# Kernel optimization log

Hardware: AMD Instinct MI355X
Metric: run time of the kernel (lower is better)

The kernel has to match this reference:

```python
import jax, jax.numpy as jnp
import numpy as np

N, S, D, H = 2048, 16, 128, 8
EPS = 1e-5  # torch.nn.LayerNorm default eps


def setup_inputs() -> dict:
    key = jax.random.key(0)
    ks = jax.random.split(key, 3)
    return {
        "x": jax.random.normal(ks[0], (N, S, D), jnp.float32),
        "Wi": jax.random.normal(ks[1], (H, S, D, D), jnp.float32),
        "Wj": jax.random.normal(ks[2], (H, S, 2 * D, D), jnp.float32),
        "ln1_w": jnp.ones((S, D), jnp.float32),
        "ln1_b": jnp.zeros((S, D), jnp.float32),
        "prelu1_a": jnp.float32(0.25),  # torch PReLU default single param
        "ln2_w": jnp.ones((H, D), jnp.float32),
        "ln2_b": jnp.zeros((H, D), jnp.float32),
        "prelu2_a": jnp.float32(0.25),
    }


def _layernorm2(x, w, b):
    # LayerNorm over the last two dims (matches torch LayerNorm([A, B]))
    mu = jnp.mean(x, axis=(-2, -1), keepdims=True)
    var = jnp.var(x, axis=(-2, -1), keepdims=True)
    return (x - mu) * jax.lax.rsqrt(var + EPS) * w + b


def _prelu(x, a):
    return jnp.where(x >= 0, x, a * x)


def reference(x, Wi, Wj, ln1_w, ln1_b, prelu1_a, ln2_w, ln2_b, prelu2_a):
    n, s, d = x.shape
    h = Wi.shape[0]
    # sort descending along source dim
    idx = jnp.argsort(-x, axis=1)                      # [N,S,D] int
    x_sort = jnp.take_along_axis(x, idx, axis=1)       # [N,S,D]
    # pad with a zero row, take adjacent differences
    pad = jnp.concatenate([x_sort, jnp.zeros((n, 1, d), x.dtype)], axis=1)
    diff = pad[:, :-1, :] - pad[:, 1:, :]              # [N,S,D]
    # positional encoding: cumsum of 2^rank / 2^S
    enc = jnp.cumsum(jnp.exp2(idx.astype(x.dtype)), axis=1) / jnp.asarray(2.0 ** s, x.dtype)
    # per-head, per-source batched matmul with Wi
    se = jnp.einsum('bsd,hsdo->bhso', enc, Wi)         # [N,H,S,D]
    se = _prelu(_layernorm2(se, ln1_w, ln1_b), prelu1_a)  # Dropout in eval mode = identity
    cat = jnp.concatenate(
        [jnp.broadcast_to(diff[:, None, :, :], (n, h, s, d)), se], axis=-1
    )                                                  # [N,H,S,2D]
    out = jnp.einsum('bhsd,hsdo->bho', cat, Wj)        # [N,H,D]
    return _prelu(_layernorm2(out, ln2_w, ln2_b), prelu2_a)
```

## Files before the change

kernel.cpp:

```cpp
#include <hip/hip_runtime.h>

#define N_ 2048
#define S_ 16
#define D_ 128
#define H_ 8
#define EPS_ 1e-5f

typedef unsigned short ushortT;
typedef unsigned int uint32;
typedef __attribute__((ext_vector_type(8))) short short8;
typedef __attribute__((ext_vector_type(8))) unsigned short ushort8;
typedef __attribute__((ext_vector_type(4))) float f32x4;
typedef __attribute__((ext_vector_type(4))) unsigned int uint4v;
typedef __attribute__((ext_vector_type(8))) float float8;

__device__ __forceinline__ ushortT f2bf(float f) {
  union { float f; uint32 u; } c; c.f = f;
  uint32 u = c.u;
  u = (u + 0x7FFFu + ((u >> 16) & 1u)) >> 16;
  return (ushortT)u;
}
__device__ __forceinline__ float bf2f(ushortT b) {
  union { uint32 u; float f; } c; c.u = ((uint32)b) << 16;
  return c.f;
}

__global__ __launch_bounds__(256) void k_prep(const float* __restrict__ x,
                                              ushortT* __restrict__ enc_sw,
                                              ushortT* __restrict__ diff_sw) {
  int g = blockIdx.x * 256 + threadIdx.x;
  int n = g >> 7, d = g & 127;
  const float* xp = x + (size_t)n * (S_ * D_) + d;
  float v[S_];
#pragma unroll
  for (int s = 0; s < S_; ++s) v[s] = xp[s * D_];
  int r[S_];
#pragma unroll
  for (int i = 0; i < S_; ++i) {
    int ri = 0;
#pragma unroll
    for (int j = 0; j < S_; ++j)
      ri += ((v[j] > v[i]) || (v[j] == v[i] && j < i)) ? 1 : 0;
    r[i] = ri;
  }
  float xs[S_ + 1];
#pragma unroll
  for (int s = 0; s < S_; ++s) {
    float acc = 0.f;
#pragma unroll
    for (int i = 0; i < S_; ++i) acc += (r[i] == s) ? v[i] : 0.f;
    xs[s] = acc;
  }
  xs[S_] = 0.f;
  int btq = n >> 7, row = n & 127;
  int wv = row >> 5, ii = (row >> 4) & 1, l15n = row & 15;
  int kkm = d >> 5, lgm = (d >> 3) & 3, em = d & 7;
  int off_nd = (((kkm * 2 + ii) * 64) + (l15n * 4 + lgm)) * 8 + em;
  int pp = d >> 6, c8p = (d >> 3) & 7, ee = d & 7;
  int q = row * 8 + (c8p ^ (row & 7));
#pragma unroll
  for (int s = 0; s < S_; ++s) {
    uint32 mm = 0;
#pragma unroll
    for (int i = 0; i < S_; ++i) mm |= (r[i] <= s) ? (1u << i) : 0u;
    enc_sw[(size_t)((btq * 16 + s) * 4 + wv) * 4096 + off_nd] =
        f2bf((float)mm * (1.f / 65536.f));
    size_t idx = ((((size_t)(btq * 16 + s) * 2 + pp) * 1024) + q) * 8 + ee;
    diff_sw[idx] = f2bf(xs[s] - xs[s + 1]);
  }
}

__global__ __launch_bounds__(512) void k_castW(const float* __restrict__ Wi,
                                               const float* __restrict__ Wj,
                                               ushortT* __restrict__ Wit_sw,
                                               ushortT* __restrict__ Wjt_sw) {
  __shared__ ushortT tile[128 * 136];
  int bx = blockIdx.x;
  int t = threadIdx.x;
  if (bx < 128) {
    int hs = bx;
    const float* src = Wi + (size_t)hs * D_ * D_;
#pragma unroll 4
    for (int i = 0; i < 32; ++i) {
      int e = t + 512 * i;
      int dd = e >> 7, o = e & 127;
      tile[dd * 136 + o] = f2bf(src[e]);
    }
    __syncthreads();
    ushortT* dst = Wit_sw + (size_t)hs * 16384;
#pragma unroll
    for (int r8 = 0; r8 < 4; ++r8) {
      int qc = r8 * 512 + t;
      int o = qc >> 4;
      int cc = (qc & 15) ^ (o & 7);
      uint4v pk;
#pragma unroll
      for (int w = 0; w < 4; ++w) {
        int d0 = cc * 8 + w * 2;
        ushortT lo = tile[d0 * 136 + o];
        ushortT hi = tile[(d0 + 1) * 136 + o];
        pk[w] = (uint32)lo | ((uint32)hi << 16);
      }
      *(uint4v*)(dst + qc * 8) = pk;
    }
  } else {
    int hs = bx - 128;
    const float* src = Wj + (size_t)hs * 256 * D_;
    for (int half = 0; half < 2; ++half) {
      if (half) __syncthreads();
#pragma unroll 4
      for (int i = 0; i < 32; ++i) {
        int e = t + 512 * i;
        int dd = e >> 7, o = e & 127;
        tile[dd * 136 + o] = f2bf(src[half * 16384 + e]);
      }
      __syncthreads();
      ushortT* dstb = Wjt_sw + ((size_t)hs * 4 + half * 2) * 8192;
#pragma unroll
      for (int r8 = 0; r8 < 4; ++r8) {
        int cg = r8 * 512 + t;
        int pl = cg >> 10;
        int qc = cg & 1023;
        int o = qc >> 3;
        int c8 = (qc & 7) ^ (o & 7);
        int dl = pl * 64 + c8 * 8;
        uint4v pk;
#pragma unroll
        for (int w = 0; w < 4; ++w) {
          ushortT lo = tile[(dl + w * 2) * 136 + o];
          ushortT hi = tile[(dl + w * 2 + 1) * 136 + o];
          pk[w] = (uint32)lo | ((uint32)hi << 16);
        }
        *(uint4v*)(dstb + (size_t)pl * 8192 + qc * 8) = pk;
      }
    }
  }
}

__global__ __launch_bounds__(256, 3) void k_gemm1(const ushortT* __restrict__ enc_sw,
                                                  const ushortT* __restrict__ Wit_sw,
                                                  ushortT* __restrict__ se,
                                                  float* __restrict__ ssum,
                                                  float* __restrict__ ssq) {
  int bt = blockIdx.x, s = blockIdx.y, h = blockIdx.z;
  __shared__ ushortT Bs[128 * 132];
  int tid = threadIdx.x;
  int wave = tid >> 6, lane = tid & 63;
  int l15 = lane & 15, lg = lane >> 4;

  const ushortT* bsrc = Wit_sw + (size_t)(h * 16 + s) * 16384;
#pragma unroll
  for (int r8 = 0; r8 < 8; ++r8)
    __builtin_amdgcn_global_load_lds(
        (const __attribute__((address_space(1))) void*)(bsrc + (r8 * 256 + tid) * 8),
        (__attribute__((address_space(3))) void*)(Bs + (r8 * 256 + wave * 64) * 8),
        16, 0, 0);

  short8 afr[4][2];
  const ushortT* abase = enc_sw + ((size_t)(bt * 16 + s) * 4 + wave) * 4096;
#pragma unroll
  for (int kk = 0; kk < 4; ++kk)
#pragma unroll
    for (int i = 0; i < 2; ++i)
      afr[kk][i] = *(const short8*)(abase + (((kk * 2 + i) * 64) + (l15 * 4 + lg)) * 8);

  __syncthreads();

  f32x4 acc[2][8];
#pragma unroll
  for (int i = 0; i < 2; ++i)
#pragma unroll
    for (int j = 0; j < 8; ++j) acc[i][j] = (f32x4)(0.f);
#pragma unroll
  for (int kk = 0; kk < 4; ++kk) {
    int cc = kk * 4 + lg;
    short8 b[8];
#pragma unroll
    for (int j = 0; j < 8; ++j) {
      int row = j * 16 + l15;
      b[j] = *(const short8*)(Bs + (row * 16 + (cc ^ (row & 7))) * 8);
    }
#pragma unroll
    for (int i = 0; i < 2; ++i)
#pragma unroll
      for (int j = 0; j < 8; ++j)
        acc[i][j] = __builtin_amdgcn_mfma_f32_16x16x32_bf16(afr[kk][i], b[j], acc[i][j], 0, 0, 0);
  }
#pragma unroll
  for (int i = 0; i < 2; ++i)
#pragma unroll
    for (int rr = 0; rr < 4; ++rr) {
      int rloc = wave * 32 + i * 16 + lg * 4 + rr;
      int b_g = bt * 128 + rloc;
      float rs = 0.f, rq = 0.f;
#pragma unroll
      for (int j = 0; j < 8; ++j) {
        float val = acc[i][j][rr];
        rs += val; rq += val * val;
      }
#pragma unroll
      for (int m = 1; m <= 8; m <<= 1) {
        rs += __shfl_xor(rs, m);
        rq += __shfl_xor(rq, m);
      }
      if (l15 == 0) {
        ssum[((size_t)s * N_ + b_g) * H_ + h] = rs;
        ssq[((size_t)s * N_ + b_g) * H_ + h] = rq;
      }
    }
  __syncthreads();
#pragma unroll
  for (int i = 0; i < 2; ++i)
#pragma unroll
    for (int rr = 0; rr < 4; ++rr) {
      int row = wave * 32 + i * 16 + lg * 4 + rr;
      int sw = (row & 7) << 3;
#pragma unroll
      for (int j = 0; j < 8; ++j) {
        int o = j * 16 + l15;
        Bs[row * 132 + (o ^ sw)] = f2bf(acc[i][j][rr]);
      }
    }
  __syncthreads();
#pragma unroll
  for (int p = 0; p < 2; ++p) {
    int row = p * 64 + (tid >> 2);
    int sw = (row & 7) << 3;
    int b_g = bt * 128 + row;
    ushortT* dst = se + (((size_t)b_g * H_ + h) * S_ + s) * D_;
#pragma unroll
    for (int qq = 0; qq < 4; ++qq) {
      int o0 = (qq * 4 + (tid & 3)) * 8;
      *(uint4v*)(dst + o0) = *(const uint4v*)(Bs + row * 132 + (o0 ^ sw));
    }
  }
}

__global__ __launch_bounds__(256) void k_finalize(const float* __restrict__ ssum,
                                                  const float* __restrict__ ssq,
                                                  float* __restrict__ mr) {
  int t = blockIdx.x * 256 + threadIdx.x;
  float s1 = 0.f, s2 = 0.f;
#pragma unroll
  for (int s = 0; s < S_; ++s) {
    s1 += ssum[(size_t)s * (N_ * H_) + t];
    s2 += ssq[(size_t)s * (N_ * H_) + t];
  }
  float mu = s1 * (1.f / 2048.f);
  float var = s2 * (1.f / 2048.f) - mu * mu;
  float rstd = rsqrtf(var + EPS_);
  mr[t * 2] = rstd;
  mr[t * 2 + 1] = -mu * rstd;
}

#define GLDS_B(DST, SRC) do {                                                 \
    const ushortT* sp_ = (SRC) + wave * 512 + lane * 8;                       \
    ushortT* dp_ = (DST) + wave * 512;                                        \
    _Pragma("unroll")                                                         \
    for (int i_ = 0; i_ < 4; ++i_)                                            \
      __builtin_amdgcn_global_load_lds(                                       \
          (const __attribute__((address_space(1))) void*)(sp_ + i_ * 2048),   \
          (__attribute__((address_space(3))) void*)(dp_ + i_ * 2048),         \
          16, 0, 0);                                                          \
  } while (0)

#define GLDS_A(DST, SRC) do {                                                 \
    const ushortT* sp_ = (SRC) + wave * 512 + lane * 8;                       \
    ushortT* dp_ = (DST) + wave * 512;                                        \
    _Pragma("unroll")                                                         \
    for (int i_ = 0; i_ < 2; ++i_)                                            \
      __builtin_amdgcn_global_load_lds(                                       \
          (const __attribute__((address_space(1))) void*)(sp_ + i_ * 2048),   \
          (__attribute__((address_space(3))) void*)(dp_ + i_ * 2048),         \
          16, 0, 0);                                                          \
  } while (0)

__global__ __launch_bounds__(256, 3) void k_gemm2(const ushortT* __restrict__ diff_sw,
                                                  const ushortT* __restrict__ se,
                                                  const ushortT* __restrict__ Wjt_sw,
                                                  const float* __restrict__ mr,
                                                  const float* __restrict__ ln1w,
                                                  const float* __restrict__ ln1b,
                                                  const float* __restrict__ pa1,
                                                  float* __restrict__ outp) {
  int bt2 = blockIdx.x, sh = blockIdx.y, h = blockIdx.z;
  int s0 = sh * 8;
  __shared__ ushortT As[2][64 * 64];
  __shared__ ushortT Bs[2][128 * 64];
  int tid = threadIdx.x;
  int wave = tid >> 6, lane = tid & 63;
  int c8 = tid & 7, trow = tid >> 3;
  int swst = ((c8 ^ (trow & 7)) * 8);
  int l15 = lane & 15, lg = lane >> 4;
  int wm = wave >> 1, wn = wave & 1;
  float a1 = pa1[0];

  float rs_r[2], nm_r[2];
  uint32 aoff_s[2];
#pragma unroll
  for (int i = 0; i < 2; ++i) {
    int row = i * 32 + trow;
    int b_g = bt2 * 64 + row;
    rs_r[i] = mr[((size_t)b_g * H_ + h) * 2];
    nm_r[i] = mr[((size_t)b_g * H_ + h) * 2 + 1];
    aoff_s[i] = ((uint32)b_g * H_ + h) * (S_ * D_) + c8 * 8;
  }
  const ushortT* dbase = diff_sw + (size_t)(bt2 >> 1) * (S_ * 2 * 8192) + (bt2 & 1) * 4096;
  ushort8 raL[2], raH[2];
  f32x4 acc[2][4];
#pragma unroll
  for (int i = 0; i < 2; ++i)
#pragma unroll
    for (int j = 0; j < 4; ++j) acc[i][j] = (f32x4)(0.f);

#define COMPUTE(XBUF) do {                                                    \
    _Pragma("unroll")                                                         \
    for (int kk = 0; kk < 2; ++kk) {                                          \
      int cc = kk * 4 + lg;                                                   \
      short8 a[2], b[4];                                                      \
      _Pragma("unroll")                                                       \
      for (int i = 0; i < 2; ++i) {                                           \
        int row = wm * 32 + i * 16 + l15;                                     \
        a[i] = *(const short8*)(As[XBUF] + row * 64 + ((cc ^ (row & 7)) * 8));\
      }                                                                       \
      _Pragma("unroll")                                                       \
      for (int j = 0; j < 4; ++j) {                                           \
        int row = wn * 64 + j * 16 + l15;                                     \
        b[j] = *(const short8*)(Bs[XBUF] + row * 64 + ((cc ^ (row & 7)) * 8));\
      }                                                                       \
      __builtin_amdgcn_s_setprio(1);                                          \
      _Pragma("unroll")                                                       \
      for (int i = 0; i < 2; ++i)                                             \
        _Pragma("unroll")                                                     \
        for (int j = 0; j < 4; ++j)                                           \
          acc[i][j] = __builtin_amdgcn_mfma_f32_16x16x32_bf16(a[i], b[j],     \
                                                              acc[i][j], 0, 0, 0); \
      __builtin_amdgcn_s_setprio(0);                                          \
    } } while (0)

#define TRANSFORM_WRITE(RA, NXBUF, SS, HALF) do {                             \
    float8 w8 = *(const float8*)(ln1w + (SS) * D_ + (HALF) * 64 + c8 * 8);    \
    float8 b8 = *(const float8*)(ln1b + (SS) * D_ + (HALF) * 64 + c8 * 8);    \
    _Pragma("unroll")                                                         \
    for (int i = 0; i < 2; ++i) {                                             \
      int row = i * 32 + trow;                                                \
      float y[8];                                                             \
      _Pragma("unroll")                                                       \
      for (int e = 0; e < 8; ++e) {                                           \
        float f = bf2f((ushortT)RA[i][e]);                                    \
        float tt = fmaf(f, rs_r[i], nm_r[i]);                                 \
        float vv = fmaf(tt, w8[e], b8[e]);                                    \
        y[e] = fmaf(a1, fminf(vv, 0.f), fmaxf(vv, 0.f));                      \
      }                                                                       \
      uint4v pk;                                                              \
      _Pragma("unroll")                                                       \
      for (int q = 0; q < 4; ++q) {                                           \
        uint32 rpk;                                                           \
        asm("v_cvt_pk_bf16_f32 %0, %1, %2" : "=v"(rpk)                        \
            : "v"(y[2 * q]), "v"(y[2 * q + 1]));                              \
        pk[q] = rpk;                                                          \
      }                                                                       \
      *(uint4v*)(As[NXBUF] + row * 64 + swst) = pk;                           \
    } } while (0)

  GLDS_A(As[0], dbase + ((size_t)s0 * 2 + 0) * 8192);
  GLDS_B(Bs[0], Wjt_sw + ((size_t)(h * 16 + s0) * 4 + 0) * 8192);
  __syncthreads();

  for (int si = 0; si < 8; ++si) {
    int s = s0 + si;
    int sn = (s + 1 < S_) ? s + 1 : 0;
#pragma unroll
    for (int i = 0; i < 2; ++i)
      raL[i] = *(const ushort8*)(se + aoff_s[i] + s * D_);
    GLDS_A(As[1], dbase + ((size_t)s * 2 + 1) * 8192);
    GLDS_B(Bs[1], Wjt_sw + ((size_t)(h * 16 + s) * 4 + 1) * 8192);
    COMPUTE(0);
    __syncthreads();
#pragma unroll
    for (int i = 0; i < 2; ++i)
      raH[i] = *(const ushort8*)(se + aoff_s[i] + s * D_ + 64);
    TRANSFORM_WRITE(raL, 0, s, 0);
    GLDS_B(Bs[0], Wjt_sw + ((size_t)(h * 16 + s) * 4 + 2) * 8192);
    COMPUTE(1);
    __syncthreads();
    TRANSFORM_WRITE(raH, 1, s, 1);
    GLDS_B(Bs[1], Wjt_sw + ((size_t)(h * 16 + s) * 4 + 3) * 8192);
    COMPUTE(0);
    __syncthreads();
    GLDS_A(As[0], dbase + ((size_t)sn * 2 + 0) * 8192);
    GLDS_B(Bs[0], Wjt_sw + ((size_t)(h * 16 + sn) * 4 + 0) * 8192);
    COMPUTE(1);
    __syncthreads();
  }

#pragma unroll
  for (int i = 0; i < 2; ++i)
#pragma unroll
    for (int j = 0; j < 4; ++j)
#pragma unroll
      for (int rr = 0; rr < 4; ++rr) {
        int b_g = bt2 * 64 + wm * 32 + i * 16 + lg * 4 + rr;
        int o = wn * 64 + j * 16 + l15;
        outp[(((size_t)sh * N_ + b_g) * H_ + h) * D_ + o] = acc[i][j][rr];
      }
}

__global__ __launch_bounds__(256) void k_ln2(const float* __restrict__ outp,
                                             const float* __restrict__ ln2w,
                                             const float* __restrict__ ln2b,
                                             const float* __restrict__ pa2,
                                             float* __restrict__ out) {
  int b = blockIdx.x, t = threadIdx.x;
  __shared__ float red[8];
  __shared__ float stats[2];
  f32x4 v = *((const f32x4*)(outp + (size_t)b * 1024) + t) +
            *((const f32x4*)(outp + (size_t)N_ * 1024 + (size_t)b * 1024) + t);
  float s1 = v[0] + v[1] + v[2] + v[3];
  float s2 = v[0] * v[0] + v[1] * v[1] + v[2] * v[2] + v[3] * v[3];
#pragma unroll
  for (int m = 1; m <= 32; m <<= 1) {
    s1 += __shfl_xor(s1, m);
    s2 += __shfl_xor(s2, m);
  }
  int wave = t >> 6, lane = t & 63;
  if (lane == 0) { red[wave] = s1; red[4 + wave] = s2; }
  __syncthreads();
  if (t == 0) {
    float S = red[0] + red[1] + red[2] + red[3];
    float Q = red[4] + red[5] + red[6] + red[7];
    float mu = S * (1.f / 1024.f);
    float var = Q * (1.f / 1024.f) - mu * mu;
    stats[0] = mu; stats[1] = rsqrtf(var + EPS_);
  }
  __syncthreads();
  float mu = stats[0], rstd = stats[1];
  float a2 = pa2[0];
  f32x4 wv = *((const f32x4*)ln2w + t);
  f32x4 bv = *((const f32x4*)ln2b + t);
  f32x4 r;
#pragma unroll
  for (int e = 0; e < 4; ++e) {
    float y = (v[e] - mu) * rstd * wv[e] + bv[e];
    r[e] = (y >= 0.f) ? y : a2 * y;
  }
  *((f32x4*)(out + (size_t)b * 1024) + t) = r;
}

extern "C" void kernel_launch(void* const* d_in, const int* in_sizes, int n_in,
                              void* d_out, int out_size, void* d_ws, size_t ws_size,
                              hipStream_t stream) {
  const float* x    = (const float*)d_in[0];
  const float* Wi   = (const float*)d_in[1];
  const float* Wj   = (const float*)d_in[2];
  const float* ln1w = (const float*)d_in[3];
  const float* ln1b = (const float*)d_in[4];
  const float* pa1  = (const float*)d_in[5];
  const float* ln2w = (const float*)d_in[6];
  const float* ln2b = (const float*)d_in[7];
  const float* pa2  = (const float*)d_in[8];
  char* ws = (char*)d_ws;
  ushortT* se      = (ushortT*)(ws + 0);
  ushortT* diff_sw = (ushortT*)(ws + 67108864);
  ushortT* Wjt_sw  = (ushortT*)(ws + 75497472);
  float*   outp    = (float*)(ws + 83886080);
  ushortT* enc_sw  = (ushortT*)(ws + 100663296);
  ushortT* Wit_sw  = (ushortT*)(ws + 109051904);
  float*   ssum    = (float*)(ws + 113246208);
  float*   ssq     = (float*)(ws + 114294784);
  float*   mr      = (float*)(ws + 115343360);
  float*   out     = (float*)d_out;

  hipLaunchKernelGGL(k_prep, dim3(1024), dim3(256), 0, stream, x, enc_sw, diff_sw);
  hipLaunchKernelGGL(k_castW, dim3(256), dim3(512), 0, stream, Wi, Wj, Wit_sw, Wjt_sw);
  hipLaunchKernelGGL(k_gemm1, dim3(16, 16, 8), dim3(256), 0, stream, enc_sw, Wit_sw, se, ssum, ssq);
  hipLaunchKernelGGL(k_finalize, dim3(64), dim3(256), 0, stream, ssum, ssq, mr);
  hipLaunchKernelGGL(k_gemm2, dim3(32, 2, 8), dim3(256), 0, stream, diff_sw, se, Wjt_sw, mr,
                     ln1w, ln1b, pa1, outp);
  hipLaunchKernelGGL(k_ln2, dim3(2048), dim3(256), 0, stream, outp, ln2w, ln2b, pa2, out);
}
```

Baseline: 183.4 us.

## Register-prefetch gemm2 operands and split S reduction into four partitions

The gemm2 kernel stops using direct global-to-LDS loads. It now prefetches the A/B tiles into registers several stages ahead and writes them to LDS after the previous compute step, which deepens the software pipeline. The source dimension is split four ways instead of two, doubling the grid to raise occupancy and parallelism. The cost is more partial-sum traffic: k_ln2 now reads four partials, and the workspace is relaid out to fit them. The register-staged buffers raise register pressure, which may limit occupancy under launch_bounds(256,3).

```diff
diff --git a/kernel.cpp b/kernel.cpp
--- a/kernel.cpp
+++ b/kernel.cpp
@@ -253,28 +253,6 @@
   mr[t * 2 + 1] = -mu * rstd;
 }
 
-#define GLDS_B(DST, SRC) do {                                                 \
-    const ushortT* sp_ = (SRC) + wave * 512 + lane * 8;                       \
-    ushortT* dp_ = (DST) + wave * 512;                                        \
-    _Pragma("unroll")                                                         \
-    for (int i_ = 0; i_ < 4; ++i_)                                            \
-      __builtin_amdgcn_global_load_lds(                                       \
-          (const __attribute__((address_space(1))) void*)(sp_ + i_ * 2048),   \
-          (__attribute__((address_space(3))) void*)(dp_ + i_ * 2048),         \
-          16, 0, 0);                                                          \
-  } while (0)
-
-#define GLDS_A(DST, SRC) do {                                                 \
-    const ushortT* sp_ = (SRC) + wave * 512 + lane * 8;                       \
-    ushortT* dp_ = (DST) + wave * 512;                                        \
-    _Pragma("unroll")                                                         \
-    for (int i_ = 0; i_ < 2; ++i_)                                            \
-      __builtin_amdgcn_global_load_lds(                                       \
-          (const __attribute__((address_space(1))) void*)(sp_ + i_ * 2048),   \
-          (__attribute__((address_space(3))) void*)(dp_ + i_ * 2048),         \
-          16, 0, 0);                                                          \
-  } while (0)
-
 __global__ __launch_bounds__(256, 3) void k_gemm2(const ushortT* __restrict__ diff_sw,
                                                   const ushortT* __restrict__ se,
                                                   const ushortT* __restrict__ Wjt_sw,
@@ -284,7 +262,7 @@
                                                   const float* __restrict__ pa1,
                                                   float* __restrict__ outp) {
   int bt2 = blockIdx.x, sh = blockIdx.y, h = blockIdx.z;
-  int s0 = sh * 8;
+  int s0 = sh * 4;
   __shared__ ushortT As[2][64 * 64];
   __shared__ ushortT Bs[2][128 * 64];
   int tid = threadIdx.x;
@@ -306,7 +284,76 @@
     aoff_s[i] = ((uint32)b_g * H_ + h) * (S_ * D_) + c8 * 8;
   }
   const ushortT* dbase = diff_sw + (size_t)(bt2 >> 1) * (S_ * 2 * 8192) + (bt2 & 1) * 4096;
-  ushort8 raL[2], raH[2];
+  const ushortT* wbase = Wjt_sw + (size_t)(h * 16) * 4 * 8192 + wave * 512 + lane * 8;
+
+  uint4v S0b0, S0b1, S0b2, S0b3, S0a0, S0a1;
+  uint4v S1b0, S1b1, S1b2, S1b3, S1a0, S1a1;
+  uint4v S2b0, S2b1, S2b2, S2b3, S2a0, S2a1;
+  uint4v S3b0, S3b1, S3b2, S3b3, S3a0, S3a1;
+
+#define ISSUE_B(P, SS, PP) do {                                               \
+    const ushortT* bp_ = wbase + ((size_t)(SS) * 4 + (PP)) * 8192;            \
+    P##b0 = *(const uint4v*)(bp_);                                            \
+    P##b1 = *(const uint4v*)(bp_ + 2048);                                     \
+    P##b2 = *(const uint4v*)(bp_ + 4096);                                     \
+    P##b3 = *(const uint4v*)(bp_ + 6144);                                     \
+  } while (0)
+
+#define ISSUE_DIFF(P, SS, PP) do {                                            \
+    ISSUE_B(P, SS, (PP));                                                     \
+    const ushortT* ap_ = dbase + ((size_t)(SS) * 2 + (PP)) * 8192 + wave * 512 + lane * 8; \
+    P##a0 = *(const uint4v*)(ap_);                                            \
+    P##a1 = *(const uint4v*)(ap_ + 2048);                                     \
+  } while (0)
+
+#define ISSUE_SE(P, SS, HALF) do {                                            \
+    ISSUE_B(P, SS, 2 + (HALF));                                               \
+    P##a0 = *(const uint4v*)(se + aoff_s[0] + (SS) * D_ + (HALF) * 64);       \
+    P##a1 = *(const uint4v*)(se + aoff_s[1] + (SS) * D_ + (HALF) * 64);       \
+  } while (0)
+
+#define WRITE_B(P, BUF) do {                                                  \
+    ushortT* dp_ = Bs[BUF] + wave * 512 + lane * 8;                           \
+    *(uint4v*)(dp_) = P##b0;                                                  \
+    *(uint4v*)(dp_ + 2048) = P##b1;                                           \
+    *(uint4v*)(dp_ + 4096) = P##b2;                                           \
+    *(uint4v*)(dp_ + 6144) = P##b3;                                           \
+  } while (0)
+
+#define WRITE_DIFF(P, BUF) do {                                               \
+    WRITE_B(P, BUF);                                                          \
+    ushortT* ap_ = As[BUF] + wave * 512 + lane * 8;                           \
+    *(uint4v*)(ap_) = P##a0;                                                  \
+    *(uint4v*)(ap_ + 2048) = P##a1;                                           \
+  } while (0)
+
+#define WRITE_SE(P, BUF, SS, HALF) do {                                       \
+    WRITE_B(P, BUF);                                                          \
+    float8 w8 = *(const float8*)(ln1w + (SS) * D_ + (HALF) * 64 + c8 * 8);    \
+    float8 b8 = *(const float8*)(ln1b + (SS) * D_ + (HALF) * 64 + c8 * 8);    \
+    _Pragma("unroll")                                                         \
+    for (int i_ = 0; i_ < 2; ++i_) {                                          \
+      ushort8 va_ = (i_ == 0) ? *(ushort8*)&P##a0 : *(ushort8*)&P##a1;        \
+      int row_ = i_ * 32 + trow;                                              \
+      float y_[8];                                                            \
+      _Pragma("unroll")                                                       \
+      for (int e_ = 0; e_ < 8; ++e_) {                                        \
+        float f_ = bf2f((ushortT)va_[e_]);                                    \
+        float t_ = fmaf(f_, rs_r[i_], nm_r[i_]);                              \
+        float v_ = fmaf(t_, w8[e_], b8[e_]);                                  \
+        y_[e_] = fmaf(a1, fminf(v_, 0.f), fmaxf(v_, 0.f));                    \
+      }                                                                       \
+      uint4v pk_;                                                             \
+      _Pragma("unroll")                                                       \
+      for (int q_ = 0; q_ < 4; ++q_) {                                        \
+        uint32 r_;                                                            \
+        asm("v_cvt_pk_bf16_f32 %0, %1, %2" : "=v"(r_)                         \
+            : "v"(y_[2 * q_]), "v"(y_[2 * q_ + 1]));                          \
+        pk_[q_] = r_;                                                         \
+      }                                                                       \
+      *(uint4v*)(As[BUF] + row_ * 64 + swst) = pk_;                           \
+    } } while (0)
+
   f32x4 acc[2][4];
 #pragma unroll
   for (int i = 0; i < 2; ++i)
@@ -338,58 +385,29 @@
       __builtin_amdgcn_s_setprio(0);                                          \
     } } while (0)
 
-#define TRANSFORM_WRITE(RA, NXBUF, SS, HALF) do {                             \
-    float8 w8 = *(const float8*)(ln1w + (SS) * D_ + (HALF) * 64 + c8 * 8);    \
-    float8 b8 = *(const float8*)(ln1b + (SS) * D_ + (HALF) * 64 + c8 * 8);    \
-    _Pragma("unroll")                                                         \
-    for (int i = 0; i < 2; ++i) {                                             \
-      int row = i * 32 + trow;                                                \
-      float y[8];                                                             \
-      _Pragma("unroll")                                                       \
-      for (int e = 0; e < 8; ++e) {                                           \
-        float f = bf2f((ushortT)RA[i][e]);                                    \
-        float tt = fmaf(f, rs_r[i], nm_r[i]);                                 \
-        float vv = fmaf(tt, w8[e], b8[e]);                                    \
-        y[e] = fmaf(a1, fminf(vv, 0.f), fmaxf(vv, 0.f));                      \
-      }                                                                       \
-      uint4v pk;                                                              \
-      _Pragma("unroll")                                                       \
-      for (int q = 0; q < 4; ++q) {                                           \
-        uint32 rpk;                                                           \
-        asm("v_cvt_pk_bf16_f32 %0, %1, %2" : "=v"(rpk)                        \
-            : "v"(y[2 * q]), "v"(y[2 * q + 1]));                              \
-        pk[q] = rpk;                                                          \
-      }                                                                       \
-      *(uint4v*)(As[NXBUF] + row * 64 + swst) = pk;                           \
-    } } while (0)
-
-  GLDS_A(As[0], dbase + ((size_t)s0 * 2 + 0) * 8192);
-  GLDS_B(Bs[0], Wjt_sw + ((size_t)(h * 16 + s0) * 4 + 0) * 8192);
+  ISSUE_DIFF(S0, s0, 0);
+  ISSUE_DIFF(S1, s0, 1);
+  ISSUE_SE(S2, s0, 0);
+  WRITE_DIFF(S0, 0);
   __syncthreads();
 
-  for (int si = 0; si < 8; ++si) {
+  for (int si = 0; si < 4; ++si) {
     int s = s0 + si;
-    int sn = (s + 1 < S_) ? s + 1 : 0;
-#pragma unroll
-    for (int i = 0; i < 2; ++i)
-      raL[i] = *(const ushort8*)(se + aoff_s[i] + s * D_);
-    GLDS_A(As[1], dbase + ((size_t)s * 2 + 1) * 8192);
-    GLDS_B(Bs[1], Wjt_sw + ((size_t)(h * 16 + s) * 4 + 1) * 8192);
+    int sn = (si + 1 < 4) ? s + 1 : s0;
+    ISSUE_SE(S3, s, 1);
+    WRITE_DIFF(S1, 1);
     COMPUTE(0);
     __syncthreads();
-#pragma unroll
-    for (int i = 0; i < 2; ++i)
-      raH[i] = *(const ushort8*)(se + aoff_s[i] + s * D_ + 64);
-    TRANSFORM_WRITE(raL, 0, s, 0);
-    GLDS_B(Bs[0], Wjt_sw + ((size_t)(h * 16 + s) * 4 + 2) * 8192);
+    ISSUE_DIFF(S0, sn, 0);
+    WRITE_SE(S2, 0, s, 0);
     COMPUTE(1);
     __syncthreads();
-    TRANSFORM_WRITE(raH, 1, s, 1);
-    GLDS_B(Bs[1], Wjt_sw + ((size_t)(h * 16 + s) * 4 + 3) * 8192);
+    ISSUE_DIFF(S1, sn, 1);
+    WRITE_SE(S3, 1, s, 1);
     COMPUTE(0);
     __syncthreads();
-    GLDS_A(As[0], dbase + ((size_t)sn * 2 + 0) * 8192);
-    GLDS_B(Bs[0], Wjt_sw + ((size_t)(h * 16 + sn) * 4 + 0) * 8192);
+    ISSUE_SE(S2, sn, 0);
+    WRITE_DIFF(S0, 0);
     COMPUTE(1);
     __syncthreads();
   }
@@ -404,6 +422,13 @@
         int o = wn * 64 + j * 16 + l15;
         outp[(((size_t)sh * N_ + b_g) * H_ + h) * D_ + o] = acc[i][j][rr];
       }
+#undef ISSUE_B
+#undef ISSUE_DIFF
+#undef ISSUE_SE
+#undef WRITE_B
+#undef WRITE_DIFF
+#undef WRITE_SE
+#undef COMPUTE
 }
 
 __global__ __launch_bounds__(256) void k_ln2(const float* __restrict__ outp,
@@ -414,8 +439,10 @@
   int b = blockIdx.x, t = threadIdx.x;
   __shared__ float red[8];
   __shared__ float stats[2];
-  f32x4 v = *((const f32x4*)(outp + (size_t)b * 1024) + t) +
-            *((const f32x4*)(outp + (size_t)N_ * 1024 + (size_t)b * 1024) + t);
+  f32x4 v = (f32x4)(0.f);
+#pragma unroll
+  for (int p = 0; p < 4; ++p)
+    v += *((const f32x4*)(outp + (size_t)p * (N_ * 1024) + (size_t)b * 1024) + t);
   float s1 = v[0] + v[1] + v[2] + v[3];
   float s2 = v[0] * v[0] + v[1] * v[1] + v[2] * v[2] + v[3] * v[3];
 #pragma unroll
@@ -464,18 +491,18 @@
   ushortT* diff_sw = (ushortT*)(ws + 67108864);
   ushortT* Wjt_sw  = (ushortT*)(ws + 75497472);
   float*   outp    = (float*)(ws + 83886080);
-  ushortT* enc_sw  = (ushortT*)(ws + 100663296);
-  ushortT* Wit_sw  = (ushortT*)(ws + 109051904);
-  float*   ssum    = (float*)(ws + 113246208);
-  float*   ssq     = (float*)(ws + 114294784);
-  float*   mr      = (float*)(ws + 115343360);
+  ushortT* enc_sw  = (ushortT*)(ws + 117440512);
+  ushortT* Wit_sw  = (ushortT*)(ws + 125829120);
+  float*   ssum    = (float*)(ws + 130023424);
+  float*   ssq     = (float*)(ws + 131072000);
+  float*   mr      = (float*)(ws + 132120576);
   float*   out     = (float*)d_out;
 
   hipLaunchKernelGGL(k_prep, dim3(1024), dim3(256), 0, stream, x, enc_sw, diff_sw);
   hipLaunchKernelGGL(k_castW, dim3(256), dim3(512), 0, stream, Wi, Wj, Wit_sw, Wjt_sw);
   hipLaunchKernelGGL(k_gemm1, dim3(16, 16, 8), dim3(256), 0, stream, enc_sw, Wit_sw, se, ssum, ssq);
   hipLaunchKernelGGL(k_finalize, dim3(64), dim3(256), 0, stream, ssum, ssq, mr);
-  hipLaunchKernelGGL(k_gemm2, dim3(32, 2, 8), dim3(256), 0, stream, diff_sw, se, Wjt_sw, mr,
+  hipLaunchKernelGGL(k_gemm2, dim3(32, 4, 8), dim3(256), 0, stream, diff_sw, se, Wjt_sw, mr,
                      ln1w, ln1b, pa1, outp);
   hipLaunchKernelGGL(k_ln2, dim3(2048), dim3(256), 0, stream, outp, ln2w, ln2b, pa2, out);
 }
```

Measured after the change: 191.3 us. 1.04x slower.
